# Kernel tuning notes

Measured on AMD Instinct MI355X. Metric: run time of the kernel, lower is better.

Reference implementation:

```python
import jax, jax.numpy as jnp
import numpy as np

TRIANGLE_TABLE = np.array([
    [-1,-1,-1,-1,-1,-1],[1,0,2,-1,-1,-1],[4,0,3,-1,-1,-1],[1,4,2,1,3,4],
    [3,1,5,-1,-1,-1],[2,3,0,2,5,3],[1,4,0,1,5,4],[4,2,5,-1,-1,-1],
    [4,5,2,-1,-1,-1],[4,1,0,4,5,1],[3,2,0,3,5,2],[1,3,5,-1,-1,-1],
    [4,1,2,4,3,1],[3,0,4,-1,-1,-1],[2,0,1,-1,-1,-1],[-1,-1,-1,-1,-1,-1]], dtype=np.int32)
NUM_TRIANGLES_TABLE = np.array([0,1,1,2,1,2,2,1,1,2,2,1,2,1,1,0], dtype=np.int32)
BASE_TET_EDGES = np.array([0,1,0,2,0,3,1,2,1,3,2,3], dtype=np.int32)


def build_tet_grid(R, scale):
    """Regular tet grid: (R+1)^3 vertices, 6 tets per cube (Kuhn split)."""
    lin = np.linspace(-1.0, 1.0, R + 1, dtype=np.float32) * scale
    X, Y, Z = np.meshgrid(lin, lin, lin, indexing='ij')
    verts = np.stack([X, Y, Z], -1).reshape(-1, 3)
    def vid(x, y, z):
        return (x * (R + 1) + y) * (R + 1) + z
    xs, ys, zs = np.meshgrid(np.arange(R), np.arange(R), np.arange(R), indexing='ij')
    offs = [(0,0,0),(1,0,0),(0,1,0),(1,1,0),(0,0,1),(1,0,1),(0,1,1),(1,1,1)]
    corners = np.stack([vid(xs+dx, ys+dy, zs+dz) for dx, dy, dz in offs], -1).reshape(-1, 8)
    KUHN = np.array([[0,1,3,7],[0,2,3,7],[0,1,5,7],[0,2,6,7],[0,4,5,7],[0,4,6,7]])
    tets = corners[:, KUHN].reshape(-1, 4).astype(np.int64)
    return verts, tets


def map_uv(face_gidx, max_idx):
    N = int(np.ceil(np.sqrt((max_idx + 1) // 2)))
    lin = jnp.linspace(0.0, 1.0 - 1.0 / N, N, dtype=jnp.float32)
    tex_y, tex_x = jnp.meshgrid(lin, lin, indexing='ij')
    pad = 0.9 / N
    uvs = jnp.stack([tex_x, tex_y, tex_x + pad, tex_y,
                     tex_x + pad, tex_y + pad, tex_x, tex_y + pad], -1).reshape(-1, 2)
    tet_idx_raw = face_gidx // 2
    tet_idx = (tet_idx_raw // N) * N + (tet_idx_raw % N)
    tri_idx = face_gidx % 2
    uv_idx = jnp.stack([tet_idx * 4, tet_idx * 4 + tri_idx + 1, tet_idx * 4 + tri_idx + 2], -1)
    return uvs, uv_idx


def marching_tets(pos_nx3, sdf_n, tet_fx4):
    occ_n = sdf_n > 0                                        # [N]
    occ_fx4 = occ_n[tet_fx4.reshape(-1)].reshape(-1, 4)      # [T,4]
    occ_sum = occ_fx4.sum(-1)
    valid_tets = (occ_sum > 0) & (occ_sum < 4)
    vt = tet_fx4[valid_tets]                                  # [Tv,4]
    all_edges = vt[:, jnp.asarray(BASE_TET_EDGES)].reshape(-1, 2)
    all_edges = jnp.sort(all_edges, axis=1)                   # matches torch sort_edges
    unique_edges, idx_map = jnp.unique(all_edges, axis=0, return_inverse=True)
    idx_map = idx_map.reshape(-1)
    mask_edges = occ_n[unique_edges].sum(-1) == 1             # surface-crossing edges
    mapping = jnp.where(mask_edges, jnp.cumsum(mask_edges) - 1, -1)
    idx_map = mapping[idx_map].reshape(-1, 6)                 # [Tv,6]
    interp_v = unique_edges[mask_edges]                       # [E,2]
    # linear interpolation of crossing point
    s = sdf_n[interp_v] * jnp.array([1.0, -1.0], sdf_n.dtype) # [E,2] = [s0,-s1]
    w = s[:, ::-1] / s.sum(1, keepdims=True)                  # [-s1, s0]/(s0-s1)
    verts = (pos_nx3[interp_v] * w[..., None]).sum(1)         # [E,3]
    # face emission via lookup tables
    v_id = jnp.array([1, 2, 4, 8])
    tetindex = (occ_fx4[valid_tets] * v_id).sum(-1)
    num_tri = jnp.asarray(NUM_TRIANGLES_TABLE)[tetindex]
    tt = jnp.asarray(TRIANGLE_TABLE)[tetindex]
    m1 = num_tri == 1
    m2 = num_tri == 2
    f1 = jnp.take_along_axis(idx_map[m1], tt[m1][:, :3], axis=1).reshape(-1, 3)
    f2 = jnp.take_along_axis(idx_map[m2], tt[m2][:, :6], axis=1).reshape(-1, 3)
    faces = jnp.concatenate([f1, f2], 0)
    num_tets = tet_fx4.shape[0]
    tet_gidx = jnp.arange(num_tets)[valid_tets]
    face_gidx = jnp.concatenate(
        [tet_gidx[m1] * 2,
         jnp.stack([tet_gidx[m2] * 2, tet_gidx[m2] * 2 + 1], -1).reshape(-1)], 0)
    uvs, uv_idx = map_uv(face_gidx, num_tets * 2)
    return verts, faces, uvs, uv_idx


def setup_inputs() -> dict:
    key = jax.random.key(0)
    k1, k2 = jax.random.split(key)
    R = 64
    verts_np, tets_np = build_tet_grid(R, 1.0)
    n = verts_np.shape[0]
    sdf = jax.random.uniform(k1, (n,), dtype=jnp.float32) - 0.1   # as in DMTetGeometry.__init__
    deform = 0.5 * jax.random.normal(k2, (n, 3), dtype=jnp.float32)
    return {
        'verts': jnp.asarray(verts_np),
        'sdf': sdf,
        'deform': deform,
        'indices': jnp.asarray(tets_np),
        'grid_res': R,
    }


def reference(verts, sdf, deform, indices, grid_res):
    v_deformed = verts + (2.0 / (grid_res * 2)) * jnp.tanh(deform)
    return marching_tets(v_deformed, sdf, indices)
```

## Files before the change

### kernel.cpp

```cpp
#include <hip/hip_runtime.h>

typedef unsigned int u32;
typedef unsigned long long u64;
typedef unsigned char u8;

__constant__ int c_tt[16][6] = {
  {-1,-1,-1,-1,-1,-1},{1,0,2,-1,-1,-1},{4,0,3,-1,-1,-1},{1,4,2,1,3,4},
  {3,1,5,-1,-1,-1},{2,3,0,2,5,3},{1,4,0,1,5,4},{4,2,5,-1,-1,-1},
  {4,5,2,-1,-1,-1},{4,1,0,4,5,1},{3,2,0,3,5,2},{1,3,5,-1,-1,-1},
  {4,1,2,4,3,1},{3,0,4,-1,-1,-1},{2,0,1,-1,-1,-1},{-1,-1,-1,-1,-1,-1}};
__constant__ int c_ntri[16] = {0,1,1,2,1,2,2,1,1,2,2,1,2,1,1,0};
__constant__ int c_kuhn[6][4] = {{0,1,3,7},{0,2,3,7},{0,1,5,7},{0,2,6,7},{0,4,5,7},{0,4,6,7}};
__constant__ int c_e0[6] = {0,0,0,1,1,2};
__constant__ int c_e1[6] = {1,2,3,2,3,3};

__device__ __forceinline__ u32 wave_incscan_u32(u32 v) {
  int lane = threadIdx.x & 63;
#pragma unroll
  for (int d = 1; d < 64; d <<= 1) {
    u32 n = __shfl_up(v, (unsigned)d, 64);
    if (lane >= d) v += n;
  }
  return v;
}
__device__ __forceinline__ u64 wave_incscan_u64(u64 v) {
  int lane = threadIdx.x & 63;
#pragma unroll
  for (int d = 1; d < 64; d <<= 1) {
    u32 lo = __shfl_up((u32)v, (unsigned)d, 64);
    u32 hi = __shfl_up((u32)(v >> 32), (unsigned)d, 64);
    u64 n = ((u64)hi << 32) | (u64)lo;
    if (lane >= d) v += n;
  }
  return v;
}
__device__ __forceinline__ u32 block_exscan_u32(u32 v, u32* wsums, u32* total) {
  int tid = threadIdx.x, lane = tid & 63, w = tid >> 6, nw = blockDim.x >> 6;
  u32 inc = wave_incscan_u32(v);
  if (lane == 63) wsums[w] = inc;
  __syncthreads();
  u32 woff = 0, tot = 0;
  for (int i = 0; i < nw; i++) { u32 s = wsums[i]; tot += s; if (i < w) woff += s; }
  __syncthreads();
  if (total) *total = tot;
  return woff + inc - v;
}
__device__ __forceinline__ u64 block_exscan_u64(u64 v, u64* wsums, u64* total) {
  int tid = threadIdx.x, lane = tid & 63, w = tid >> 6, nw = blockDim.x >> 6;
  u64 inc = wave_incscan_u64(v);
  if (lane == 63) wsums[w] = inc;
  __syncthreads();
  u64 woff = 0, tot = 0;
  for (int i = 0; i < nw; i++) { u64 s = wsums[i]; tot += s; if (i < w) woff += s; }
  __syncthreads();
  if (total) *total = tot;
  return woff + inc - v;
}

template <int CR>
__global__ __launch_bounds__(256) void kA(const float* __restrict__ sdf, u32* __restrict__ lpack,
                                          u8* __restrict__ tcode, u32* __restrict__ bsumV,
                                          u32* __restrict__ bsumT, int NV, int T, int nvb, int rr) {
  const int R = CR ? CR : rr;
  const int R1 = R + 1, R1sq = R1 * R1;
  __shared__ u32 ws[4];
  int tid = threadIdx.x, bid = blockIdx.x;
  if (bid < nvb) {
    int v = bid * 256 + tid;
    u32 m = 0;
    if (v < NV) {
      int z = v % R1, tq = v / R1, y = tq % R1, x = tq / R1;
      bool o = sdf[v] > 0.0f;
      bool bx = x < R, by = y < R, bz = z < R;
      if (bz && (sdf[v + 1] > 0.0f) != o) m |= 1;
      if (by && (sdf[v + R1] > 0.0f) != o) m |= 2;
      if (by && bz && (sdf[v + R1 + 1] > 0.0f) != o) m |= 4;
      if (bx && (sdf[v + R1sq] > 0.0f) != o) m |= 8;
      if (bx && bz && (sdf[v + R1sq + 1] > 0.0f) != o) m |= 16;
      if (bx && by && (sdf[v + R1sq + R1] > 0.0f) != o) m |= 32;
      if (bx && by && bz && (sdf[v + R1sq + R1 + 1] > 0.0f) != o) m |= 64;
    }
    u32 tot;
    u32 ex = block_exscan_u32(__popc(m), ws, &tot);
    if (v < NV) lpack[v] = (ex << 7) | m;
    if (tid == 0) bsumV[bid] = tot;
  } else {
    int t = (bid - nvb) * 256 + tid;
    u32 packed = 0;
    if (t < T) {
      int c = t / 6, k = t - 6 * c;
      int z = c % R, tq = c / R, y = tq % R, x = tq / R;
      int v000 = (x * R1 + y) * R1 + z;
      int coff[8] = {0, R1sq, R1, R1sq + R1, 1, R1sq + 1, R1 + 1, R1sq + R1 + 1};
      int code = 0;
#pragma unroll
      for (int j = 0; j < 4; j++)
        code |= (sdf[v000 + coff[c_kuhn[k][j]]] > 0.0f ? 1 : 0) << j;
      tcode[t] = (u8)code;
      int n = c_ntri[code];
      packed = (n == 1 ? 1u : 0u) | (n == 2 ? (1u << 16) : 0u);
    }
    u32 tot;
    block_exscan_u32(packed, ws, &tot);
    if (tid == 0) bsumT[bid - nvb] = tot;
  }
}

__global__ __launch_bounds__(1024) void kC(const u32* __restrict__ bsumV, u32* __restrict__ boffV,
                                           int nvb, const u32* __restrict__ bsumT,
                                           u64* __restrict__ boffT, int ntb, u32* __restrict__ hdr) {
  if (blockIdx.x == 0) {
    __shared__ u32 ws32[16];
    u32 carry = 0;
    for (int base = 0; base < nvb; base += 1024) {
      int i = base + threadIdx.x;
      u32 v = (i < nvb) ? bsumV[i] : 0;
      u32 tot;
      u32 ex = block_exscan_u32(v, ws32, &tot);
      if (i < nvb) boffV[i] = carry + ex;
      carry += tot;
    }
    if (threadIdx.x == 0) hdr[0] = carry;
  } else {
    __shared__ u64 ws64[16];
    u64 carry = 0;
    for (int base = 0; base < ntb; base += 1024) {
      int i = base + threadIdx.x;
      u32 p = (i < ntb) ? bsumT[i] : 0;
      u64 v = (u64)(p & 0xffffu) | ((u64)(p >> 16) << 32);
      u64 tot;
      u64 ex = block_exscan_u64(v, ws64, &tot);
      if (i < ntb) boffT[i] = carry + ex;
      carry += tot;
    }
    if (threadIdx.x == 0) { hdr[1] = (u32)carry; hdr[2] = (u32)(carry >> 32); }
  }
}

template <int CR, int CNU>
__global__ __launch_bounds__(256) void kD(const float* __restrict__ verts, const float* __restrict__ sdf,
                                          const float* __restrict__ deform, const u32* __restrict__ lpack,
                                          const u32* __restrict__ boffV, const u8* __restrict__ tcode,
                                          const u64* __restrict__ boffT, const u32* __restrict__ hdr,
                                          float* __restrict__ out, int NV, int T, int nvb, int nuvb,
                                          int rr, int nuu, float sdefs, double inv) {
  const int R = CR ? CR : rr;
  const int R1 = R + 1, R1sq = R1 * R1;
  const u32 NU = CNU ? CNU : (u32)nuu;
  __shared__ u32 ws[4];
  int tid = threadIdx.x, bid = blockIdx.x;
  if (bid < nuvb) {
    u32 chunk = (u32)bid * 256 + tid;
    u32 E = hdr[0], F = hdr[1] + 2u * hdr[2];
    size_t A = (size_t)3 * E + (size_t)3 * F;
    u32 sh = (u32)(A & 3);
    size_t A4 = A - sh;
    u32 total = 8u * NU * NU;
    int e0 = (int)(4u * chunk) - (int)sh;
    if (e0 >= (int)total) return;
    float padf = (float)(0.9 * inv);
    float vals[4];
    bool ok[4];
    bool all4 = true;
#pragma unroll
    for (int j = 0; j < 4; j++) {
      int e = e0 + j;
      bool valid = (e >= 0) && (e < (int)total);
      ok[j] = valid;
      all4 &= valid;
      float val = 0.0f;
      if (valid) {
        u32 cell = (u32)e >> 3;
        int comp = e & 7;
        u32 row = cell / NU, col = cell - row * NU;
        float b = (comp & 1) ? (float)((double)row * inv) : (float)((double)col * inv);
        bool addp = (comp == 2) | (comp == 4) | (comp == 5) | (comp == 7);
        val = addp ? b + padf : b;
      }
      vals[j] = val;
    }
    size_t basef = A4 + 4 * (size_t)chunk;
    if (all4) {
      *(float4*)(out + basef) = make_float4(vals[0], vals[1], vals[2], vals[3]);
    } else {
#pragma unroll
      for (int j = 0; j < 4; j++)
        if (ok[j]) out[basef + j] = vals[j];
    }
  } else if (bid < nuvb + nvb) {
    int vb = bid - nuvb;
    int v = vb * 256 + tid;
    if (v >= NV) return;
    u32 pv = lpack[v];
    u32 m = pv & 0x7fu;
    if (!m) return;
    u32 r = boffV[vb] + (pv >> 7);
    int deltas[7] = {1, R1, R1 + 1, R1sq, R1sq + 1, R1sq + R1, R1sq + R1 + 1};
    float sa = sdf[v];
    float pa0 = verts[3 * v + 0] + sdefs * tanhf(deform[3 * v + 0]);
    float pa1 = verts[3 * v + 1] + sdefs * tanhf(deform[3 * v + 1]);
    float pa2 = verts[3 * v + 2] + sdefs * tanhf(deform[3 * v + 2]);
#pragma unroll
    for (int k = 0; k < 7; k++) {
      if ((m >> k) & 1) {
        int b = v + deltas[k];
        float sb = sdf[b];
        float den = sa - sb;
        float w0 = -sb / den, w1 = sa / den;
        float pb0 = verts[3 * b + 0] + sdefs * tanhf(deform[3 * b + 0]);
        float pb1 = verts[3 * b + 1] + sdefs * tanhf(deform[3 * b + 1]);
        float pb2 = verts[3 * b + 2] + sdefs * tanhf(deform[3 * b + 2]);
        out[3 * r + 0] = pa0 * w0 + pb0 * w1;
        out[3 * r + 1] = pa1 * w0 + pb1 * w1;
        out[3 * r + 2] = pa2 * w0 + pb2 * w1;
        r++;
      }
    }
  } else {
    int tb = bid - nuvb - nvb;
    int t = tb * 256 + tid;
    int code = (t < T) ? (int)tcode[t] : 0;
    int n = c_ntri[code];
    u32 packed = (n == 1 ? 1u : 0u) | (n == 2 ? (1u << 16) : 0u);
    u32 ex = block_exscan_u32(packed, ws, nullptr);
    if (t >= T || n == 0) return;
    u64 bo = boffT[tb];
    u32 s1 = (u32)bo + (ex & 0xffffu);
    u32 s2 = (u32)(bo >> 32) + (ex >> 16);
    u32 E = hdr[0], F1 = hdr[1], F2 = hdr[2];
    u32 F = F1 + 2u * F2;
    size_t fb = (size_t)3 * E;
    size_t ub = fb + (size_t)3 * F + (size_t)8 * NU * NU;
    int c = t / 6, k = t - 6 * c;
    int z = c % R, tq = c / R, y = tq % R, x = tq / R;
    int v000 = (x * R1 + y) * R1 + z;
    int coff[8] = {0, R1sq, R1, R1sq + R1, 1, R1sq + 1, R1 + 1, R1sq + R1 + 1};
    int g4 = 4 * t;
    for (int tri = 0; tri < n; tri++) {
      u32 row = (n == 1) ? s1 : (F1 + 2u * s2 + (u32)tri);
#pragma unroll
      for (int j = 0; j < 3; j++) {
        int slot = c_tt[code][3 * tri + j];
        int ci = c_kuhn[k][c_e0[slot]], cj = c_kuhn[k][c_e1[slot]];
        int oa = coff[ci], ob = coff[cj];
        int lo = oa < ob ? oa : ob;
        int d = oa < ob ? ob - oa : oa - ob;
        int va = v000 + lo;
        int dx = d >= R1sq ? 1 : 0; d -= dx * R1sq;
        int dy = d >= R1 ? 1 : 0;   d -= dy * R1;
        int kb = (dx << 2) + (dy << 1) + d - 1;
        u32 pv = lpack[va];
        u32 fidx = boffV[va >> 8] + (pv >> 7) + __popc(pv & 0x7fu & ((1u << kb) - 1u));
        out[fb + 3 * row + j] = (float)fidx;
      }
      out[ub + 3 * row + 0] = (float)g4;
      out[ub + 3 * row + 1] = (float)(g4 + tri + 1);
      out[ub + 3 * row + 2] = (float)(g4 + tri + 2);
    }
  }
}

extern "C" void kernel_launch(void* const* d_in, const int* in_sizes, int n_in,
                              void* d_out, int out_size, void* d_ws, size_t ws_size,
                              hipStream_t stream) {
  const float* verts = (const float*)d_in[0];
  const float* sdf = (const float*)d_in[1];
  const float* deform = (const float*)d_in[2];
  int NV = in_sizes[0] / 3;
  int T = in_sizes[3] / 4;
  int R = 1;
  while ((long long)(R + 1) * (R + 1) * (R + 1) < (long long)NV) R++;
  int NU = 1;
  while ((long long)NU * NU < (long long)T) NU++;
  int nvb = (NV + 255) / 256;
  int ntb = (T + 255) / 256;
  long long nchunks = (8LL * NU * NU) / 4 + 2;
  int nuvb = (int)((nchunks + 255) / 256);

  char* w = (char*)d_ws;
  u64* boffT = (u64*)w; w += (size_t)ntb * 8;
  u32* bsumV = (u32*)w; w += (size_t)nvb * 4;
  u32* boffV = (u32*)w; w += (size_t)nvb * 4;
  u32* bsumT = (u32*)w; w += (size_t)ntb * 4;
  u32* lpack = (u32*)w; w += (size_t)nvb * 256 * 4;
  u32* hdr = (u32*)w;   w += 64;
  u8* tcode = (u8*)w;   w += (size_t)T;

  float sdefs = 2.0f / (float)(R * 2);
  double inv = 1.0 / (double)NU;
  float* outf = (float*)d_out;

  if (R == 64 && NU == 1255) {
    kA<64><<<dim3(nvb + ntb), dim3(256), 0, stream>>>(sdf, lpack, tcode, bsumV, bsumT, NV, T, nvb, R);
    kC<<<dim3(2), dim3(1024), 0, stream>>>(bsumV, boffV, nvb, bsumT, boffT, ntb, hdr);
    kD<64, 1255><<<dim3(nuvb + nvb + ntb), dim3(256), 0, stream>>>(
        verts, sdf, deform, lpack, boffV, tcode, boffT, hdr, outf,
        NV, T, nvb, nuvb, R, NU, sdefs, inv);
  } else {
    kA<0><<<dim3(nvb + ntb), dim3(256), 0, stream>>>(sdf, lpack, tcode, bsumV, bsumT, NV, T, nvb, R);
    kC<<<dim3(2), dim3(1024), 0, stream>>>(bsumV, boffV, nvb, bsumT, boffT, ntb, hdr);
    kD<0, 0><<<dim3(nuvb + nvb + ntb), dim3(256), 0, stream>>>(
        verts, sdf, deform, lpack, boffV, tcode, boffT, hdr, outf,
        NV, T, nvb, nuvb, R, NU, sdefs, inv);
  }
}
```

Baseline: 150.2 us.

## Precompute deformed positions, per-cube tet codes with packed local offsets, widen UV writes

Result: faster. 136.5 us (-9.1%).

```diff
diff --git a/kernel.cpp b/kernel.cpp
--- a/kernel.cpp
+++ b/kernel.cpp
@@ -58,9 +58,11 @@
 }
 
 template <int CR>
-__global__ __launch_bounds__(256) void kA(const float* __restrict__ sdf, u32* __restrict__ lpack,
-                                          u8* __restrict__ tcode, u32* __restrict__ bsumV,
-                                          u32* __restrict__ bsumT, int NV, int T, int nvb, int rr) {
+__global__ __launch_bounds__(256) void kA(const float* __restrict__ sdf, const float* __restrict__ verts,
+                                          const float* __restrict__ deform, float4* __restrict__ pos4,
+                                          u32* __restrict__ lpack, u32* __restrict__ tpack,
+                                          u32* __restrict__ bsumV, u32* __restrict__ bsumT,
+                                          int NV, int Tc, int nvb, int rr, float sdefs) {
   const int R = CR ? CR : rr;
   const int R1 = R + 1, R1sq = R1 * R1;
   __shared__ u32 ws[4];
@@ -68,9 +70,11 @@
   if (bid < nvb) {
     int v = bid * 256 + tid;
     u32 m = 0;
+    float s = 0.0f;
     if (v < NV) {
       int z = v % R1, tq = v / R1, y = tq % R1, x = tq / R1;
-      bool o = sdf[v] > 0.0f;
+      s = sdf[v];
+      bool o = s > 0.0f;
       bool bx = x < R, by = y < R, bz = z < R;
       if (bz && (sdf[v + 1] > 0.0f) != o) m |= 1;
       if (by && (sdf[v + R1] > 0.0f) != o) m |= 2;
@@ -82,33 +86,62 @@
     }
     u32 tot;
     u32 ex = block_exscan_u32(__popc(m), ws, &tot);
-    if (v < NV) lpack[v] = (ex << 7) | m;
+    if (v < NV) {
+      lpack[v] = (ex << 7) | m;
+      float4 p;
+      p.x = verts[3 * v + 0] + sdefs * tanhf(deform[3 * v + 0]);
+      p.y = verts[3 * v + 1] + sdefs * tanhf(deform[3 * v + 1]);
+      p.z = verts[3 * v + 2] + sdefs * tanhf(deform[3 * v + 2]);
+      p.w = s;
+      pos4[v] = p;
+    }
     if (tid == 0) bsumV[bid] = tot;
   } else {
-    int t = (bid - nvb) * 256 + tid;
-    u32 packed = 0;
-    if (t < T) {
-      int c = t / 6, k = t - 6 * c;
+    int bid2 = bid - nvb;
+    int c = bid2 * 256 + tid;
+    u32 pk = 0;
+    u32 b = 0;
+    int codes[6];
+    if (c < Tc) {
       int z = c % R, tq = c / R, y = tq % R, x = tq / R;
       int v000 = (x * R1 + y) * R1 + z;
       int coff[8] = {0, R1sq, R1, R1sq + R1, 1, R1sq + 1, R1 + 1, R1sq + R1 + 1};
-      int code = 0;
-#pragma unroll
-      for (int j = 0; j < 4; j++)
-        code |= (sdf[v000 + coff[c_kuhn[k][j]]] > 0.0f ? 1 : 0) << j;
-      tcode[t] = (u8)code;
-      int n = c_ntri[code];
-      packed = (n == 1 ? 1u : 0u) | (n == 2 ? (1u << 16) : 0u);
+#pragma unroll
+      for (int j = 0; j < 8; j++) b |= (sdf[v000 + coff[j]] > 0.0f ? 1u : 0u) << j;
+#pragma unroll
+      for (int k = 0; k < 6; k++) {
+        int code = ((b >> c_kuhn[k][0]) & 1) | (((b >> c_kuhn[k][1]) & 1) << 1) |
+                   (((b >> c_kuhn[k][2]) & 1) << 2) | (((b >> c_kuhn[k][3]) & 1) << 3);
+        codes[k] = code;
+        int n = c_ntri[code];
+        pk += (n == 1 ? 1u : 0u) + (n == 2 ? (1u << 16) : 0u);
+      }
     }
     u32 tot;
-    block_exscan_u32(packed, ws, &tot);
-    if (tid == 0) bsumT[bid - nvb] = tot;
+    u32 ex = block_exscan_u32(pk, ws, &tot);
+    if (c < Tc) {
+      u32 r1 = ex & 0xffffu, r2 = ex >> 16;
+      u32 tp[6];
+#pragma unroll
+      for (int k = 0; k < 6; k++) {
+        int code = codes[k];
+        tp[k] = (u32)code | (r1 << 4) | (r2 << 15);
+        int n = c_ntri[code];
+        r1 += (n == 1);
+        r2 += (n == 2);
+      }
+      u32* dst = tpack + 6 * c;
+      *(uint2*)(dst + 0) = make_uint2(tp[0], tp[1]);
+      *(uint2*)(dst + 2) = make_uint2(tp[2], tp[3]);
+      *(uint2*)(dst + 4) = make_uint2(tp[4], tp[5]);
+    }
+    if (tid == 0) bsumT[bid2] = tot;
   }
 }
 
 __global__ __launch_bounds__(1024) void kC(const u32* __restrict__ bsumV, u32* __restrict__ boffV,
                                            int nvb, const u32* __restrict__ bsumT,
-                                           u64* __restrict__ boffT, int ntb, u32* __restrict__ hdr) {
+                                           u64* __restrict__ boffT, int ncb, u32* __restrict__ hdr) {
   if (blockIdx.x == 0) {
     __shared__ u32 ws32[16];
     u32 carry = 0;
@@ -124,13 +157,13 @@
   } else {
     __shared__ u64 ws64[16];
     u64 carry = 0;
-    for (int base = 0; base < ntb; base += 1024) {
+    for (int base = 0; base < ncb; base += 1024) {
       int i = base + threadIdx.x;
-      u32 p = (i < ntb) ? bsumT[i] : 0;
+      u32 p = (i < ncb) ? bsumT[i] : 0;
       u64 v = (u64)(p & 0xffffu) | ((u64)(p >> 16) << 32);
       u64 tot;
       u64 ex = block_exscan_u64(v, ws64, &tot);
-      if (i < ntb) boffT[i] = carry + ex;
+      if (i < ncb) boffT[i] = carry + ex;
       carry += tot;
     }
     if (threadIdx.x == 0) { hdr[1] = (u32)carry; hdr[2] = (u32)(carry >> 32); }
@@ -138,54 +171,52 @@
 }
 
 template <int CR, int CNU>
-__global__ __launch_bounds__(256) void kD(const float* __restrict__ verts, const float* __restrict__ sdf,
-                                          const float* __restrict__ deform, const u32* __restrict__ lpack,
-                                          const u32* __restrict__ boffV, const u8* __restrict__ tcode,
+__global__ __launch_bounds__(256) void kD(const float4* __restrict__ pos4, const u32* __restrict__ lpack,
+                                          const u32* __restrict__ boffV, const u32* __restrict__ tpack,
                                           const u64* __restrict__ boffT, const u32* __restrict__ hdr,
                                           float* __restrict__ out, int NV, int T, int nvb, int nuvb,
-                                          int rr, int nuu, float sdefs, double inv) {
+                                          int rr, int nuu, double inv) {
   const int R = CR ? CR : rr;
   const int R1 = R + 1, R1sq = R1 * R1;
   const u32 NU = CNU ? CNU : (u32)nuu;
-  __shared__ u32 ws[4];
   int tid = threadIdx.x, bid = blockIdx.x;
+  u32 E = hdr[0], F1 = hdr[1], F2 = hdr[2];
+  u32 F = F1 + 2u * F2;
+  size_t fb = (size_t)3 * E;
+  size_t A = fb + (size_t)3 * F;
+  size_t ub = A + (size_t)8 * NU * NU;
   if (bid < nuvb) {
     u32 chunk = (u32)bid * 256 + tid;
-    u32 E = hdr[0], F = hdr[1] + 2u * hdr[2];
-    size_t A = (size_t)3 * E + (size_t)3 * F;
     u32 sh = (u32)(A & 3);
-    size_t A4 = A - sh;
-    u32 total = 8u * NU * NU;
-    int e0 = (int)(4u * chunk) - (int)sh;
-    if (e0 >= (int)total) return;
+    int totalf = (int)(8u * NU * NU);
+    int e0 = (int)(8u * chunk) - (int)sh;
+    if (e0 >= totalf) return;
     float padf = (float)(0.9 * inv);
-    float vals[4];
-    bool ok[4];
-    bool all4 = true;
-#pragma unroll
-    for (int j = 0; j < 4; j++) {
-      int e = e0 + j;
-      bool valid = (e >= 0) && (e < (int)total);
-      ok[j] = valid;
-      all4 &= valid;
-      float val = 0.0f;
-      if (valid) {
-        u32 cell = (u32)e >> 3;
-        int comp = e & 7;
-        u32 row = cell / NU, col = cell - row * NU;
-        float b = (comp & 1) ? (float)((double)row * inv) : (float)((double)col * inv);
-        bool addp = (comp == 2) | (comp == 4) | (comp == 5) | (comp == 7);
-        val = addp ? b + padf : b;
-      }
-      vals[j] = val;
-    }
-    size_t basef = A4 + 4 * (size_t)chunk;
-    if (all4) {
-      *(float4*)(out + basef) = make_float4(vals[0], vals[1], vals[2], vals[3]);
+    u32 row1 = chunk / NU, col1 = chunk - row1 * NU;
+    u32 col0 = (col1 == 0) ? (NU - 1) : (col1 - 1);
+    u32 row0 = (col1 == 0) ? (row1 - 1) : row1;
+    float x1 = (float)((double)col1 * inv), y1 = (float)((double)row1 * inv);
+    float xp1 = x1 + padf, yp1 = y1 + padf;
+    float x0 = (float)((double)col0 * inv), y0 = (float)((double)row0 * inv);
+    float xp0 = x0 + padf, yp0 = y0 + padf;
+    (void)xp0;
+    float vals[8];
+    switch (sh) {
+      case 0: vals[0]=x1; vals[1]=y1; vals[2]=xp1; vals[3]=y1; vals[4]=xp1; vals[5]=yp1; vals[6]=x1; vals[7]=yp1; break;
+      case 1: vals[0]=yp0; vals[1]=x1; vals[2]=y1; vals[3]=xp1; vals[4]=y1; vals[5]=xp1; vals[6]=yp1; vals[7]=x1; break;
+      case 2: vals[0]=x0; vals[1]=yp0; vals[2]=x1; vals[3]=y1; vals[4]=xp1; vals[5]=y1; vals[6]=xp1; vals[7]=yp1; break;
+      default: vals[0]=yp0; vals[1]=x0; vals[2]=yp0; vals[3]=x1; vals[4]=y1; vals[5]=xp1; vals[6]=y1; vals[7]=xp1; break;
+    }
+    size_t basef = (A - sh) + 8 * (size_t)chunk;
+    if (e0 >= 0 && e0 + 7 < totalf) {
+      *(float4*)(out + basef)     = make_float4(vals[0], vals[1], vals[2], vals[3]);
+      *(float4*)(out + basef + 4) = make_float4(vals[4], vals[5], vals[6], vals[7]);
     } else {
 #pragma unroll
-      for (int j = 0; j < 4; j++)
-        if (ok[j]) out[basef + j] = vals[j];
+      for (int j = 0; j < 8; j++) {
+        int e = e0 + j;
+        if (e >= 0 && e < totalf) out[basef + j] = vals[j];
+      }
     }
   } else if (bid < nuvb + nvb) {
     int vb = bid - nuvb;
@@ -196,41 +227,30 @@
     if (!m) return;
     u32 r = boffV[vb] + (pv >> 7);
     int deltas[7] = {1, R1, R1 + 1, R1sq, R1sq + 1, R1sq + R1, R1sq + R1 + 1};
-    float sa = sdf[v];
-    float pa0 = verts[3 * v + 0] + sdefs * tanhf(deform[3 * v + 0]);
-    float pa1 = verts[3 * v + 1] + sdefs * tanhf(deform[3 * v + 1]);
-    float pa2 = verts[3 * v + 2] + sdefs * tanhf(deform[3 * v + 2]);
+    float4 a4 = pos4[v];
 #pragma unroll
     for (int k = 0; k < 7; k++) {
       if ((m >> k) & 1) {
-        int b = v + deltas[k];
-        float sb = sdf[b];
-        float den = sa - sb;
-        float w0 = -sb / den, w1 = sa / den;
-        float pb0 = verts[3 * b + 0] + sdefs * tanhf(deform[3 * b + 0]);
-        float pb1 = verts[3 * b + 1] + sdefs * tanhf(deform[3 * b + 1]);
-        float pb2 = verts[3 * b + 2] + sdefs * tanhf(deform[3 * b + 2]);
-        out[3 * r + 0] = pa0 * w0 + pb0 * w1;
-        out[3 * r + 1] = pa1 * w0 + pb1 * w1;
-        out[3 * r + 2] = pa2 * w0 + pb2 * w1;
+        float4 b4 = pos4[v + deltas[k]];
+        float den = a4.w - b4.w;
+        float w0 = -b4.w / den, w1 = a4.w / den;
+        out[3 * r + 0] = a4.x * w0 + b4.x * w1;
+        out[3 * r + 1] = a4.y * w0 + b4.y * w1;
+        out[3 * r + 2] = a4.z * w0 + b4.z * w1;
         r++;
       }
     }
   } else {
     int tb = bid - nuvb - nvb;
     int t = tb * 256 + tid;
-    int code = (t < T) ? (int)tcode[t] : 0;
+    if (t >= T) return;
+    u32 tp = tpack[t];
+    int code = (int)(tp & 0xfu);
     int n = c_ntri[code];
-    u32 packed = (n == 1 ? 1u : 0u) | (n == 2 ? (1u << 16) : 0u);
-    u32 ex = block_exscan_u32(packed, ws, nullptr);
-    if (t >= T || n == 0) return;
-    u64 bo = boffT[tb];
-    u32 s1 = (u32)bo + (ex & 0xffffu);
-    u32 s2 = (u32)(bo >> 32) + (ex >> 16);
-    u32 E = hdr[0], F1 = hdr[1], F2 = hdr[2];
-    u32 F = F1 + 2u * F2;
-    size_t fb = (size_t)3 * E;
-    size_t ub = fb + (size_t)3 * F + (size_t)8 * NU * NU;
+    if (n == 0) return;
+    u64 bo = boffT[tb / 6];
+    u32 s1 = (u32)bo + ((tp >> 4) & 0x7ffu);
+    u32 s2 = (u32)(bo >> 32) + ((tp >> 15) & 0x7ffu);
     int c = t / 6, k = t - 6 * c;
     int z = c % R, tq = c / R, y = tq % R, x = tq / R;
     int v000 = (x * R1 + y) * R1 + z;
@@ -272,35 +292,38 @@
   while ((long long)(R + 1) * (R + 1) * (R + 1) < (long long)NV) R++;
   int NU = 1;
   while ((long long)NU * NU < (long long)T) NU++;
+  int Tc = T / 6;
   int nvb = (NV + 255) / 256;
+  int ncb = (Tc + 255) / 256;
   int ntb = (T + 255) / 256;
-  long long nchunks = (8LL * NU * NU) / 4 + 2;
+  long long nchunks = (long long)NU * NU + 1;
   int nuvb = (int)((nchunks + 255) / 256);
 
   char* w = (char*)d_ws;
-  u64* boffT = (u64*)w; w += (size_t)ntb * 8;
+  float4* pos4 = (float4*)w; w += (size_t)nvb * 256 * 16;
+  u64* boffT = (u64*)w; w += (size_t)ncb * 8;
+  u32* tpack = (u32*)w; w += (size_t)T * 4;
   u32* bsumV = (u32*)w; w += (size_t)nvb * 4;
   u32* boffV = (u32*)w; w += (size_t)nvb * 4;
-  u32* bsumT = (u32*)w; w += (size_t)ntb * 4;
+  u32* bsumT = (u32*)w; w += (size_t)ncb * 4;
   u32* lpack = (u32*)w; w += (size_t)nvb * 256 * 4;
   u32* hdr = (u32*)w;   w += 64;
-  u8* tcode = (u8*)w;   w += (size_t)T;
 
   float sdefs = 2.0f / (float)(R * 2);
   double inv = 1.0 / (double)NU;
   float* outf = (float*)d_out;
 
   if (R == 64 && NU == 1255) {
-    kA<64><<<dim3(nvb + ntb), dim3(256), 0, stream>>>(sdf, lpack, tcode, bsumV, bsumT, NV, T, nvb, R);
-    kC<<<dim3(2), dim3(1024), 0, stream>>>(bsumV, boffV, nvb, bsumT, boffT, ntb, hdr);
+    kA<64><<<dim3(nvb + ncb), dim3(256), 0, stream>>>(sdf, verts, deform, pos4, lpack, tpack,
+                                                      bsumV, bsumT, NV, Tc, nvb, R, sdefs);
+    kC<<<dim3(2), dim3(1024), 0, stream>>>(bsumV, boffV, nvb, bsumT, boffT, ncb, hdr);
     kD<64, 1255><<<dim3(nuvb + nvb + ntb), dim3(256), 0, stream>>>(
-        verts, sdf, deform, lpack, boffV, tcode, boffT, hdr, outf,
-        NV, T, nvb, nuvb, R, NU, sdefs, inv);
+        pos4, lpack, boffV, tpack, boffT, hdr, outf, NV, T, nvb, nuvb, R, NU, inv);
   } else {
-    kA<0><<<dim3(nvb + ntb), dim3(256), 0, stream>>>(sdf, lpack, tcode, bsumV, bsumT, NV, T, nvb, R);
-    kC<<<dim3(2), dim3(1024), 0, stream>>>(bsumV, boffV, nvb, bsumT, boffT, ntb, hdr);
+    kA<0><<<dim3(nvb + ncb), dim3(256), 0, stream>>>(sdf, verts, deform, pos4, lpack, tpack,
+                                                     bsumV, bsumT, NV, Tc, nvb, R, sdefs);
+    kC<<<dim3(2), dim3(1024), 0, stream>>>(bsumV, boffV, nvb, bsumT, boffT, ncb, hdr);
     kD<0, 0><<<dim3(nuvb + nvb + ntb), dim3(256), 0, stream>>>(
-        verts, sdf, deform, lpack, boffV, tcode, boffT, hdr, outf,
-        NV, T, nvb, nuvb, R, NU, sdefs, inv);
-  }
-}
+        pos4, lpack, boffV, tpack, boffT, hdr, outf, NV, T, nvb, nuvb, R, NU, inv);
+  }
+}
```
